# Optimization experiments

Measured on AMD Instinct MI355X. Metric: run time of the kernel, lower is better.

The kernel has to match this reference:

```python
import jax, jax.numpy as jnp
import numpy as np
import math

B, S, D, H, F = 4, 1024, 1024, 16, 4096
NUM_BUCKETS, MAX_DISTANCE = 32, 128
LN_EPS = 1e-5


def _relative_position_bucket(relative_position, num_buckets=NUM_BUCKETS, max_distance=MAX_DISTANCE):
    # bidirectional T5 bucketing, faithful to the torch source
    n = -relative_position
    num_buckets = num_buckets // 2  # 16
    ret = (n < 0).astype(jnp.int32) * num_buckets
    n = jnp.abs(n)
    max_exact = num_buckets // 2  # 8
    is_small = n < max_exact
    val_if_large = max_exact + (
        jnp.log(jnp.maximum(n, 1).astype(jnp.float32) / max_exact)
        / math.log(max_distance / max_exact)
        * (num_buckets - max_exact)
    ).astype(jnp.int32)
    val_if_large = jnp.minimum(val_if_large, num_buckets - 1)
    return ret + jnp.where(is_small, n, val_if_large)


def layer_norm(x, g, b):
    mu = jnp.mean(x, axis=-1, keepdims=True)
    var = jnp.mean((x - mu) ** 2, axis=-1, keepdims=True)
    return g * (x - mu) / jnp.sqrt(var + LN_EPS) + b


def setup_inputs() -> dict:
    key = jax.random.key(0)
    ks = jax.random.split(key, 12)
    s = 0.02
    return {
        "in_state": jax.random.normal(ks[0], (B, S, D), jnp.float32),
        "padding_mask": jnp.ones((B, S), jnp.int32),
        "Wq": jax.random.normal(ks[1], (D, D), jnp.float32) * s,
        "bq": jnp.zeros((D,), jnp.float32),
        "Wk": jax.random.normal(ks[2], (D, D), jnp.float32) * s,
        "bk": jnp.zeros((D,), jnp.float32),
        "Wv": jax.random.normal(ks[3], (D, D), jnp.float32) * s,
        "bv": jnp.zeros((D,), jnp.float32),
        "Wo": jax.random.normal(ks[4], (D, D), jnp.float32) * s,
        "bo": jnp.zeros((D,), jnp.float32),
        "rel_bias": jax.random.normal(ks[5], (NUM_BUCKETS, H), jnp.float32) * s,
        "ln1_g": jnp.ones((D,), jnp.float32),
        "ln1_b": jnp.zeros((D,), jnp.float32),
        "W1": jax.random.normal(ks[6], (D, F), jnp.float32) * s,
        "b1": jnp.zeros((F,), jnp.float32),
        "W2": jax.random.normal(ks[7], (F, D), jnp.float32) * s,
        "b2": jnp.zeros((D,), jnp.float32),
        "ln2_g": jnp.ones((D,), jnp.float32),
        "ln2_b": jnp.zeros((D,), jnp.float32),
    }


def reference(in_state, padding_mask, Wq, bq, Wk, bk, Wv, bv, Wo, bo, rel_bias,
              ln1_g, ln1_b, W1, b1, W2, b2, ln2_g, ln2_b):
    b, s, d = in_state.shape
    dh = d // H
    q = in_state @ Wq + bq
    k = in_state @ Wk + bk
    v = in_state @ Wv + bv
    # faithful to torch's q.view(B*H, S, d_head) flat reshape (no head transpose)
    qh = q.reshape(b * H, s, dh)
    kh = k.reshape(b * H, s, dh)
    vh = v.reshape(b * H, s, dh)
    scores = jnp.einsum('bqd,bkd->bqk', qh, kh)  # no 1/sqrt(d) scaling (T5 style)
    # relative position bias: [H, S, S] tiled over batch -> block index b*H+h gets head h
    rel_pos = jnp.arange(s)[:, None] - jnp.arange(s)[None, :]
    buckets = _relative_position_bucket(rel_pos)
    bias = rel_bias[buckets].transpose(2, 0, 1)  # [H, S, S]
    bias = jnp.tile(bias, (b, 1, 1))  # [B*H, S, S]
    # padding mask: log(0/1) -> -inf/0; block b*H+h uses mask[b, value_index]
    pad = jnp.log(padding_mask.astype(jnp.float32))  # [B, S]
    pad = jnp.repeat(pad, H, axis=0)[:, None, :]  # [B*H, 1, S]
    attw = jax.nn.softmax(scores + bias + pad, axis=-1)
    att = (attw @ vh).reshape(b, s, d)
    att = att @ Wo + bo
    h = layer_norm(att + in_state, ln1_g, ln1_b)
    ff = jnp.maximum(h @ W1 + b1, 0.0) @ W2 + b2
    out = layer_norm(ff + h, ln2_g, ln2_b)
    return out
```

## Files before the change

### kernel.cpp

```cpp
#include <hip/hip_runtime.h>
#include <hip/hip_bf16.h>

typedef unsigned short u16;
typedef __attribute__((ext_vector_type(8))) short bhalf8;
typedef __attribute__((ext_vector_type(4))) float f32x4;

#define DEV __device__ __forceinline__

DEV float bf2f(u16 u) { union { unsigned int i; float f; } c; c.i = ((unsigned int)u) << 16; return c.f; }
DEV u16 f2bf(float f) {
  union { float f; unsigned int i; } c; c.f = f;
  unsigned int x = c.i;
  x += 0x7fffu + ((x >> 16) & 1u);
  return (u16)(x >> 16);
}

DEV void async16(const void* g, void* l) {
  __builtin_amdgcn_global_load_lds((__attribute__((address_space(1))) void*)g,
                                   (__attribute__((address_space(3))) void*)l, 16, 0, 0);
}

struct Ptr11 { const void* p[11]; };
struct TC4 { const void* in[4]; u16* out[4]; };

__global__ void detect_kernel(const unsigned int* __restrict__ x, int* __restrict__ flag) {
  int t = threadIdx.x;
  int cnt = 0;
  for (int i = t; i < 256; i += 64) {
    unsigned int w = x[i];
    int e = (w >> 7) & 0xFF;
    if (e >= 96 && e <= 134) cnt++;
  }
#pragma unroll
  for (int o = 1; o < 64; o <<= 1) cnt += __shfl_xor(cnt, o, 64);
  if (t == 0) *flag = (cnt >= 192) ? 1 : 0;
}

DEV bhalf8 load8B(const void* base, size_t e, int isbf) {
  if (isbf) return *(const bhalf8*)((const u16*)base + e);
  const float* f = (const float*)base + e;
  float4 a = *(const float4*)f;
  float4 b = *(const float4*)(f + 4);
  bhalf8 r;
  r[0] = (short)f2bf(a.x); r[1] = (short)f2bf(a.y); r[2] = (short)f2bf(a.z); r[3] = (short)f2bf(a.w);
  r[4] = (short)f2bf(b.x); r[5] = (short)f2bf(b.y); r[6] = (short)f2bf(b.z); r[7] = (short)f2bf(b.w);
  return r;
}

__global__ __launch_bounds__(256) void convert_x(const void* __restrict__ x,
                                                 u16* __restrict__ dst,
                                                 const int* __restrict__ flag) {
  int c = blockIdx.x * 256 + threadIdx.x;
  u16* d = dst + (size_t)c * 4;
  if (*flag) {
    *(ushort4*)d = ((const ushort4*)x)[c];
  } else {
    float4 v = ((const float4*)x)[c];
    d[0] = f2bf(v.x); d[1] = f2bf(v.y); d[2] = f2bf(v.z); d[3] = f2bf(v.w);
  }
}

__global__ __launch_bounds__(256) void convert_small(Ptr11 s, float* __restrict__ dst,
                                                     const int* __restrict__ flag) {
  const int isbf = *flag;
  const int SZ[11] = {1024,1024,1024,1024,512,1024,1024,4096,1024,1024,1024};
  for (int i = threadIdx.x; i < 13824; i += 256) {
    int acc = 0, seg = -1, off = 0;
#pragma unroll
    for (int s2 = 0; s2 < 11; ++s2) {
      if (seg < 0 && i < acc + SZ[s2]) { seg = s2; off = i - acc; }
      acc += SZ[s2];
    }
    dst[i] = isbf ? bf2f(((const u16*)s.p[seg])[off]) : ((const float*)s.p[seg])[off];
  }
}

DEV void tconv_tile(const void* in, u16* out, int R, int C, int isbf) {
  __shared__ __align__(16) u16 tile[64][72];
  const int t = threadIdx.x;
  const int c0 = blockIdx.x * 64, r0 = blockIdx.y * 64;
#pragma unroll
  for (int r = 0; r < 2; ++r) {
    int idx = r * 256 + t;
    int ri = idx >> 3, cc = (idx & 7) * 8;
    bhalf8 v = load8B(in, (size_t)(r0 + ri) * C + c0 + cc, isbf);
    *(bhalf8*)(&tile[ri][cc]) = v;
  }
  __syncthreads();
#pragma unroll
  for (int r = 0; r < 2; ++r) {
    int idx = r * 256 + t;
    int co = idx >> 3, rc = (idx & 7) * 8;
    bhalf8 v;
#pragma unroll
    for (int ii = 0; ii < 8; ++ii) v[ii] = (short)tile[rc + ii][co];
    *(bhalf8*)(out + (size_t)(c0 + co) * R + r0 + rc) = v;
  }
}

__global__ __launch_bounds__(256) void tconv_w4(TC4 p, const int* __restrict__ flag) {
  int z = blockIdx.z;
  tconv_tile(p.in[z], p.out[z], 1024, 1024, *flag);
}

__global__ __launch_bounds__(256) void tconv_generic(const void* in, u16* out, int R, int C,
                                                     const int* __restrict__ flag) {
  tconv_tile(in, out, R, C, *flag);
}

__global__ __launch_bounds__(256) void transpose_generic(const u16* in, u16* out, int R, int C) {
  __shared__ __align__(16) u16 tile[64][72];
  const int t = threadIdx.x;
  const int c0 = blockIdx.x * 64, r0 = blockIdx.y * 64;
  size_t bs = (size_t)R * C * blockIdx.z;
#pragma unroll
  for (int r = 0; r < 2; ++r) {
    int idx = r * 256 + t;
    int ri = idx >> 3, cc = (idx & 7) * 8;
    *(bhalf8*)(&tile[ri][cc]) = *(const bhalf8*)(in + bs + (size_t)(r0 + ri) * C + c0 + cc);
  }
  __syncthreads();
#pragma unroll
  for (int r = 0; r < 2; ++r) {
    int idx = r * 256 + t;
    int co = idx >> 3, rc = (idx & 7) * 8;
    bhalf8 v;
#pragma unroll
    for (int ii = 0; ii < 8; ++ii) v[ii] = (short)tile[rc + ii][co];
    *(bhalf8*)(out + bs + (size_t)(c0 + co) * R + r0 + rc) = v;
  }
}

#define MFMA_BF16(a, b, c) __builtin_amdgcn_mfma_f32_16x16x32_bf16(a, b, c, 0, 0, 0)

template<int RELU>
__global__ __launch_bounds__(512) void gemm256(
    const u16* __restrict__ A, const u16* __restrict__ BT0,
    const float* __restrict__ b0, const float* __restrict__ b1, const float* __restrict__ b2,
    u16* __restrict__ C0, int M, int N, int K, long sBT, long sC)
{
  __shared__ __align__(16) u16 ldsAll[65536];
  (void)M;

  const int t = threadIdx.x;
  const int wv = t >> 6, l = t & 63;
  const int wm = wv >> 2, wn = wv & 3;
  const int m0 = blockIdx.y * 256, n0 = blockIdx.x * 256;
  const int z = blockIdx.z;

  const u16* BT = BT0 + (long)z * sBT;
  const float* bias = (z == 0) ? b0 : (z == 1 ? b1 : b2);
  u16* C = C0 + (long)z * sC;

  const int ri = t >> 3;
  const int slc8 = (((t & 7) ^ (ri & 7)) << 3);
  const u16* agp = A + (size_t)(m0 + ri) * K + slc8;
  const int rB = ((ri >> 5) << 6) | (ri & 31);
  const u16* bgp = BT + (size_t)(n0 + rB) * K + slc8;

  char* lbase = (char*)ldsAll;
  char* ldst = lbase + wv * 1024;

#define STG_A(bufb, h, j, kt) async16(agp + (size_t)((j) * 128 + (h) * 64) * K + (size_t)(kt) * 64, \
                                      ldst + (bufb) * 32768 + (h) * 16384 + (j) * 8192)
#define STG_B(bufb, h, j, kt) async16(bgp + (size_t)((j) * 128 + (h) * 32) * K + (size_t)(kt) * 64, \
                                      ldst + 65536 + (bufb) * 32768 + (h) * 16384 + (j) * 8192)

  int offA[4][2], offB[2][2];
#pragma unroll
  for (int mi = 0; mi < 4; ++mi)
#pragma unroll
    for (int s = 0; s < 2; ++s)
      offA[mi][s] = wm * 8192 + (mi * 16 + (l & 15)) * 128 + ((((s << 2) + (l >> 4)) ^ (l & 7)) << 4);
#pragma unroll
  for (int nj = 0; nj < 2; ++nj)
#pragma unroll
    for (int s = 0; s < 2; ++s)
      offB[nj][s] = 65536 + wn * 4096 + (nj * 16 + (l & 15)) * 128 + ((((s << 2) + (l >> 4)) ^ (l & 7)) << 4);

  const int NT = K >> 6;
  f32x4 acc[8][4] = {};

  STG_A(0, 0, 0, 0); STG_A(0, 0, 1, 0);
  STG_B(0, 0, 0, 0); STG_B(0, 0, 1, 0);
  STG_B(0, 1, 0, 0); STG_B(0, 1, 1, 0);
  STG_A(0, 1, 0, 0); STG_A(0, 1, 1, 0);
  if (NT > 1) {
    STG_A(1, 0, 0, 1); STG_A(1, 0, 1, 1);
    STG_B(1, 0, 0, 1); STG_B(1, 0, 1, 1);
    STG_B(1, 1, 0, 1); STG_B(1, 1, 1, 1);
    asm volatile("s_waitcnt vmcnt(6)" ::: "memory");
  } else {
    asm volatile("s_waitcnt vmcnt(0)" ::: "memory");
  }
  __builtin_amdgcn_s_barrier();

  for (int tt = 0; tt < NT; ++tt) {
    const int bf = tt & 1;
    const int bo = bf << 15;
    bhalf8 af[4][2], p0[2][2], p1[2][2];

#pragma unroll
    for (int mi = 0; mi < 4; ++mi)
#pragma unroll
      for (int s = 0; s < 2; ++s)
        af[mi][s] = *(const bhalf8*)(lbase + bo + offA[mi][s]);
#pragma unroll
    for (int nj = 0; nj < 2; ++nj)
#pragma unroll
      for (int s = 0; s < 2; ++s)
        p0[nj][s] = *(const bhalf8*)(lbase + bo + offB[nj][s]);
    if (tt + 1 < NT) { STG_A(bf ^ 1, 1, 0, tt + 1); STG_A(bf ^ 1, 1, 1, tt + 1); }
    __builtin_amdgcn_s_barrier();
    asm volatile("s_waitcnt lgkmcnt(0)" ::: "memory");
    __builtin_amdgcn_s_setprio(1);
#pragma unroll
    for (int mi = 0; mi < 4; ++mi)
#pragma unroll
      for (int nj = 0; nj < 2; ++nj) {
        acc[mi][nj] = MFMA_BF16(af[mi][0], p0[nj][0], acc[mi][nj]);
        acc[mi][nj] = MFMA_BF16(af[mi][1], p0[nj][1], acc[mi][nj]);
      }
    __builtin_amdgcn_s_setprio(0);
    __builtin_amdgcn_s_barrier();

#pragma unroll
    for (int nj = 0; nj < 2; ++nj)
#pragma unroll
      for (int s = 0; s < 2; ++s)
        p1[nj][s] = *(const bhalf8*)(lbase + bo + 16384 + offB[nj][s]);
    if (tt + 2 < NT) { STG_A(bf, 0, 0, tt + 2); STG_A(bf, 0, 1, tt + 2); }
    __builtin_amdgcn_s_barrier();
    asm volatile("s_waitcnt lgkmcnt(0)" ::: "memory");
    __builtin_amdgcn_s_setprio(1);
#pragma unroll
    for (int mi = 0; mi < 4; ++mi)
#pragma unroll
      for (int nj = 0; nj < 2; ++nj) {
        acc[mi][2 + nj] = MFMA_BF16(af[mi][0], p1[nj][0], acc[mi][2 + nj]);
        acc[mi][2 + nj] = MFMA_BF16(af[mi][1], p1[nj][1], acc[mi][2 + nj]);
      }
    __builtin_amdgcn_s_setprio(0);
    __builtin_amdgcn_s_barrier();

#pragma unroll
    for (int mi = 0; mi < 4; ++mi)
#pragma unroll
      for (int s = 0; s < 2; ++s)
        af[mi][s] = *(const bhalf8*)(lbase + bo + 16384 + offA[mi][s]);
    if (tt + 2 < NT) { STG_B(bf, 0, 0, tt + 2); STG_B(bf, 0, 1, tt + 2); }
    __builtin_amdgcn_s_barrier();
    asm volatile("s_waitcnt lgkmcnt(0)" ::: "memory");
    __builtin_amdgcn_s_setprio(1);
#pragma unroll
    for (int mi = 0; mi < 4; ++mi)
#pragma unroll
      for (int nj = 0; nj < 2; ++nj) {
        acc[4 + mi][2 + nj] = MFMA_BF16(af[mi][0], p1[nj][0], acc[4 + mi][2 + nj]);
        acc[4 + mi][2 + nj] = MFMA_BF16(af[mi][1], p1[nj][1], acc[4 + mi][2 + nj]);
      }
    __builtin_amdgcn_s_setprio(0);
    __builtin_amdgcn_s_barrier();

    if (tt + 2 < NT) { STG_B(bf, 1, 0, tt + 2); STG_B(bf, 1, 1, tt + 2); }
    __builtin_amdgcn_s_barrier();
    __builtin_amdgcn_s_setprio(1);
#pragma unroll
    for (int mi = 0; mi < 4; ++mi)
#pragma unroll
      for (int nj = 0; nj < 2; ++nj) {
        acc[4 + mi][nj] = MFMA_BF16(af[mi][0], p0[nj][0], acc[4 + mi][nj]);
        acc[4 + mi][nj] = MFMA_BF16(af[mi][1], p0[nj][1], acc[4 + mi][nj]);
      }
    __builtin_amdgcn_s_setprio(0);
    if (tt < NT - 2) {
      asm volatile("s_waitcnt vmcnt(6)" ::: "memory");
    } else if (tt == NT - 2) {
      asm volatile("s_waitcnt vmcnt(0)" ::: "memory");
    }
    __builtin_amdgcn_s_barrier();
  }
#undef STG_A
#undef STG_B

  const int lr = (l >> 4) << 2, lcc = l & 15;
#pragma unroll
  for (int nj = 0; nj < 4; ++nj) {
    int col = n0 + wn * 64 + nj * 16 + lcc;
    float bb = bias[col];
#pragma unroll
    for (int mi = 0; mi < 8; ++mi) {
#pragma unroll
      for (int r = 0; r < 4; ++r) {
        int row = m0 + wm * 128 + mi * 16 + lr + r;
        float v = acc[mi][nj][r] + bb;
        if (RELU) v = fmaxf(v, 0.0f);
        C[(size_t)row * N + col] = f2bf(v);
      }
    }
  }
}

template<int RELU>
__global__ __launch_bounds__(512) void gemm_bt(
    const u16* __restrict__ A, const u16* __restrict__ BT0,
    const float* __restrict__ b0, const float* __restrict__ b1, const float* __restrict__ b2,
    u16* __restrict__ C0, int M, int N, int K, long sBT, long sC)
{
  __shared__ __align__(16) u16 ldsA[128 * 32];
  __shared__ __align__(16) u16 ldsB[128 * 32];

  const int t = threadIdx.x;
  const int wv = t >> 6, l = t & 63;
  const int wm = wv >> 2, wn = wv & 3;
  const int m0 = blockIdx.y * 128, n0 = blockIdx.x * 128;
  const int z = blockIdx.z;

  const u16* BT = BT0 + (long)z * sBT;
  const float* bias = (z == 0) ? b0 : (z == 1 ? b1 : b2);
  u16* C = C0 + (long)z * sC;

  const int mm_s = t >> 2, kc_s = (t & 3) ^ ((t >> 4) & 3);
  const u16* agp = A + (size_t)(m0 + mm_s) * K + kc_s * 8;
  const u16* bgp = BT + (size_t)(n0 + mm_s) * K + kc_s * 8;
  char* la = (char*)ldsA + wv * 1024;
  char* lb = (char*)ldsB + wv * 1024;

  int a_off[4], b_off[2];
#pragma unroll
  for (int i = 0; i < 4; ++i) {
    int mm = wm * 64 + i * 16 + (l & 15);
    a_off[i] = (mm * 4 + ((l >> 4) ^ ((mm >> 2) & 3))) * 8;
  }
#pragma unroll
  for (int j = 0; j < 2; ++j) {
    int nn = wn * 32 + j * 16 + (l & 15);
    b_off[j] = (nn * 4 + ((l >> 4) ^ ((nn >> 2) & 3))) * 8;
  }

  f32x4 acc[4][2] = {};

  for (int kt = 0; kt < K; kt += 32) {
    __syncthreads();
    async16(agp + kt, la);
    async16(bgp + kt, lb);
    __syncthreads();

    bhalf8 af[4], bfr[2];
#pragma unroll
    for (int i = 0; i < 4; ++i) af[i] = *(const bhalf8*)(ldsA + a_off[i]);
#pragma unroll
    for (int j = 0; j < 2; ++j) bfr[j] = *(const bhalf8*)(ldsB + b_off[j]);
#pragma unroll
    for (int mi = 0; mi < 4; ++mi)
#pragma unroll
      for (int nj = 0; nj < 2; ++nj)
        acc[mi][nj] = __builtin_amdgcn_mfma_f32_16x16x32_bf16(af[mi], bfr[nj], acc[mi][nj], 0, 0, 0);
  }

  const int lr = (l >> 4) << 2, lc = l & 15;
#pragma unroll
  for (int nj = 0; nj < 2; ++nj) {
    int col = n0 + wn * 32 + nj * 16 + lc;
    float bb = bias[col];
#pragma unroll
    for (int mi = 0; mi < 4; ++mi) {
#pragma unroll
      for (int r = 0; r < 4; ++r) {
        int row = m0 + wm * 64 + mi * 16 + lr + r;
        float v = acc[mi][nj][r] + bb;
        if (RELU) v = fmaxf(v, 0.0f);
        C[(size_t)row * N + col] = f2bf(v);
      }
    }
  }
}

template<int RELU>
__global__ __launch_bounds__(256) void gemm_bn(
    const u16* __restrict__ A, const void* __restrict__ B,
    const float* __restrict__ bias, u16* __restrict__ C, int M, int N, int K,
    const int* __restrict__ flag)
{
  __shared__ __align__(16) u16 ldsA[128][40];
  __shared__ __align__(16) u16 ldsB[128][40];

  const int isbf = *flag;
  const int t = threadIdx.x;
  const int wv = t >> 6, l = t & 63;
  const int wm = wv & 1, wn = wv >> 1;
  const int m0 = blockIdx.y * 128, n0 = blockIdx.x * 128;

  const int srow = t >> 1, scol = (t & 1) * 16;
  const u16* agp = A + (size_t)(m0 + srow) * K + scol;

  const int kk = t >> 3;
  const int nn = (t & 7) * 16;

  f32x4 acc[4][4] = {};

  for (int kt = 0; kt < K; kt += 32) {
    bhalf8 a0 = *(const bhalf8*)(agp + kt);
    bhalf8 a1 = *(const bhalf8*)(agp + kt + 8);
    size_t e0 = (size_t)(kt + kk) * N + n0 + nn;
    bhalf8 b0v = load8B(B, e0, isbf);
    bhalf8 b1v = load8B(B, e0 + 8, isbf);
    __syncthreads();
    *(bhalf8*)(&ldsA[srow][scol])     = a0;
    *(bhalf8*)(&ldsA[srow][scol + 8]) = a1;
#pragma unroll
    for (int j = 0; j < 8; ++j) ldsB[nn + j][kk]     = (u16)b0v[j];
#pragma unroll
    for (int j = 0; j < 8; ++j) ldsB[nn + 8 + j][kk] = (u16)b1v[j];
    __syncthreads();

    bhalf8 af[4], bfr[4];
#pragma unroll
    for (int i = 0; i < 4; ++i)
      af[i] = *(const bhalf8*)(&ldsA[wm * 64 + i * 16 + (l & 15)][(l >> 4) * 8]);
#pragma unroll
    for (int i = 0; i < 4; ++i)
      bfr[i] = *(const bhalf8*)(&ldsB[wn * 64 + i * 16 + (l & 15)][(l >> 4) * 8]);
#pragma unroll
    for (int mi = 0; mi < 4; ++mi)
#pragma unroll
      for (int ni = 0; ni < 4; ++ni)
        acc[mi][ni] = __builtin_amdgcn_mfma_f32_16x16x32_bf16(af[mi], bfr[ni], acc[mi][ni], 0, 0, 0);
  }

  const int lr = (l >> 4) << 2, lc = l & 15;
#pragma unroll
  for (int ni = 0; ni < 4; ++ni) {
    int col = n0 + wn * 64 + ni * 16 + lc;
    float bb = bias[col];
#pragma unroll
    for (int mi = 0; mi < 4; ++mi) {
#pragma unroll
      for (int r = 0; r < 4; ++r) {
        int row = m0 + wm * 64 + mi * 16 + lr + r;
        float v = acc[mi][ni][r] + bb;
        if (RELU) v = fmaxf(v, 0.0f);
        C[(size_t)row * N + col] = f2bf(v);
      }
    }
  }
}

__global__ __launch_bounds__(256) void lut_kernel(const float* __restrict__ rbc, float* __restrict__ lut) {
  int idx = blockIdx.x * 256 + threadIdx.x;
  if (idx >= 16 * 2047) return;
  int h = idx / 2047;
  int dp = idx - h * 2047;
  int delta = dp - 1023;
  int n = -delta;
  int ret = 0;
  if (n < 0) { ret = 16; n = -n; }
  int bkt;
  if (n < 8) bkt = n;
  else {
    float v = logf((float)n * 0.125f) / logf(16.0f) * 8.0f;
    bkt = 8 + (int)v;
    if (bkt > 15) bkt = 15;
  }
  lut[idx] = (rbc[(ret + bkt) * 16 + h] - 12.0f) * 1.44269504f;
}

__global__ __launch_bounds__(256) void attn_fused(
    const u16* __restrict__ q, const u16* __restrict__ k, const u16* __restrict__ vt,
    const int* __restrict__ mask, const float* __restrict__ lut, u16* __restrict__ att)
{
  __shared__ __align__(16) u16 ldsQ[64][72];
  __shared__ __align__(16) u16 ldsK[64][72];
  __shared__ __align__(16) u16 ldsV[64][72];
  __shared__ __align__(16) u16 ldsP[4][16][72];
  __shared__ float ldsLut[2047];
  __shared__ float ldsPad[64];

  const int t = threadIdx.x;
  const int wv = t >> 6, l = t & 63;
  const int bh = blockIdx.x, qt = blockIdx.y;
  const int b = bh >> 4, h = bh & 15;
  const size_t base = (size_t)bh * 65536;
  const int q0 = qt * 64;

  for (int i = t; i < 2047; i += 256) ldsLut[i] = lut[h * 2047 + i];

  const int sr = t >> 2, sc = (t & 3) * 16;
  {
    bhalf8 q0v = *(const bhalf8*)(q + base + (size_t)(q0 + sr) * 64 + sc);
    bhalf8 q1v = *(const bhalf8*)(q + base + (size_t)(q0 + sr) * 64 + sc + 8);
    *(bhalf8*)(&ldsQ[sr][sc])     = q0v;
    *(bhalf8*)(&ldsQ[sr][sc + 8]) = q1v;
  }
  __syncthreads();

  bhalf8 qf[2];
  {
    int mm = wv * 16 + (l & 15);
#pragma unroll
    for (int s = 0; s < 2; ++s)
      qf[s] = *(const bhalf8*)(&ldsQ[mm][s * 32 + (l >> 4) * 8]);
  }

  float ls_part[4] = {0.0f, 0.0f, 0.0f, 0.0f};
  f32x4 acc_o[4] = {};

  const int* mrow = mask + b * 1024;

  for (int kt = 0; kt < 16; ++kt) {
    const int k0 = kt * 64;
    bhalf8 k0v = *(const bhalf8*)(k + base + (size_t)(k0 + sr) * 64 + sc);
    bhalf8 k1v = *(const bhalf8*)(k + base + (size_t)(k0 + sr) * 64 + sc + 8);
    bhalf8 v0v = *(const bhalf8*)(vt + base + (size_t)sr * 1024 + k0 + sc);
    bhalf8 v1v = *(const bhalf8*)(vt + base + (size_t)sr * 1024 + k0 + sc + 8);
    __syncthreads();
    *(bhalf8*)(&ldsK[sr][sc])     = k0v;
    *(bhalf8*)(&ldsK[sr][sc + 8]) = k1v;
    *(bhalf8*)(&ldsV[sr][sc])     = v0v;
    *(bhalf8*)(&ldsV[sr][sc + 8]) = v1v;
    if (t < 64) {
      int mv = mrow[k0 + t];
      ldsPad[t] = (mv > 0) ? __log2f((float)mv) : -1e30f;
    }
    __syncthreads();

    f32x4 accS[4] = {};
#pragma unroll
    for (int s = 0; s < 2; ++s) {
#pragma unroll
      for (int ni = 0; ni < 4; ++ni) {
        int nnj = ni * 16 + (l & 15);
        bhalf8 kf = *(const bhalf8*)(&ldsK[nnj][s * 32 + (l >> 4) * 8]);
        accS[ni] = __builtin_amdgcn_mfma_f32_16x16x32_bf16(qf[s], kf, accS[ni], 0, 0, 0);
      }
    }

    float padv[4];
#pragma unroll
    for (int ni = 0; ni < 4; ++ni) padv[ni] = ldsPad[ni * 16 + (l & 15)];
    const int ib = q0 + wv * 16 + ((l >> 4) << 2);
#pragma unroll
    for (int r = 0; r < 4; ++r) {
      int i_l = ((l >> 4) << 2) + r;
#pragma unroll
      for (int ni = 0; ni < 4; ++ni) {
        int j_l = ni * 16 + (l & 15);
        float s = fmaf(accS[ni][r], 1.44269504f, ldsLut[(ib + r) - (k0 + j_l) + 1023]) + padv[ni];
        float p = exp2f(s);
        ls_part[r] += p;
        ldsP[wv][i_l][j_l] = f2bf(p);
      }
    }

#pragma unroll
    for (int s = 0; s < 2; ++s) {
      int mm = l & 15;
      bhalf8 pf = *(const bhalf8*)(&ldsP[wv][mm][s * 32 + (l >> 4) * 8]);
#pragma unroll
      for (int ni = 0; ni < 4; ++ni) {
        int e = ni * 16 + (l & 15);
        bhalf8 vf = *(const bhalf8*)(&ldsV[e][s * 32 + (l >> 4) * 8]);
        acc_o[ni] = __builtin_amdgcn_mfma_f32_16x16x32_bf16(pf, vf, acc_o[ni], 0, 0, 0);
      }
    }
  }

#pragma unroll
  for (int r = 0; r < 4; ++r) {
#pragma unroll
    for (int off = 1; off < 16; off <<= 1) ls_part[r] += __shfl_xor(ls_part[r], off, 64);
    ls_part[r] = 1.0f / ls_part[r];
  }

#pragma unroll
  for (int ni = 0; ni < 4; ++ni) {
#pragma unroll
    for (int r = 0; r < 4; ++r) {
      int i = q0 + wv * 16 + ((l >> 4) << 2) + r;
      int e = ni * 16 + (l & 15);
      att[base + (size_t)i * 64 + e] = f2bf(acc_o[ni][r] * ls_part[r]);
    }
  }
}

template<int LAST>
__global__ __launch_bounds__(256) void ln_kernel(
    const u16* __restrict__ x, const u16* __restrict__ res,
    const float* __restrict__ g, const float* __restrict__ b,
    void* __restrict__ out, const int* __restrict__ flag)
{
  const int row = blockIdx.x, t = threadIdx.x;
  const size_t off = (size_t)row * 1024 + t * 4;
  ushort4 xv = *(const ushort4*)(x + off);
  ushort4 rv = *(const ushort4*)(res + off);
  float v0 = bf2f(xv.x) + bf2f(rv.x);
  float v1 = bf2f(xv.y) + bf2f(rv.y);
  float v2 = bf2f(xv.z) + bf2f(rv.z);
  float v3 = bf2f(xv.w) + bf2f(rv.w);
  float s = v0 + v1 + v2 + v3;
  float sq = v0 * v0 + v1 * v1 + v2 * v2 + v3 * v3;
#pragma unroll
  for (int o = 1; o < 64; o <<= 1) { s += __shfl_xor(s, o, 64); sq += __shfl_xor(sq, o, 64); }
  __shared__ float red[8];
  const int wv = t >> 6, l = t & 63;
  if (l == 0) { red[wv] = s; red[4 + wv] = sq; }
  __syncthreads();
  s = red[0] + red[1] + red[2] + red[3];
  sq = red[4] + red[5] + red[6] + red[7];
  float mu = s * 0.0009765625f;
  float var = sq * 0.0009765625f - mu * mu;
  float rstd = rsqrtf(var + 1e-5f);
  float4 gv = *(const float4*)(g + t * 4);
  float4 bv = *(const float4*)(b + t * 4);
  float o0 = gv.x * (v0 - mu) * rstd + bv.x;
  float o1 = gv.y * (v1 - mu) * rstd + bv.y;
  float o2 = gv.z * (v2 - mu) * rstd + bv.z;
  float o3 = gv.w * (v3 - mu) * rstd + bv.w;
  if (!LAST) {
    ushort4 ov; ov.x = f2bf(o0); ov.y = f2bf(o1); ov.z = f2bf(o2); ov.w = f2bf(o3);
    *(ushort4*)((u16*)out + off) = ov;
  } else {
    if (*flag) {
      ushort4 ov; ov.x = f2bf(o0); ov.y = f2bf(o1); ov.z = f2bf(o2); ov.w = f2bf(o3);
      *(ushort4*)((u16*)out + off) = ov;
    } else {
      float4 ov; ov.x = o0; ov.y = o1; ov.z = o2; ov.w = o3;
      *(float4*)((float*)out + off) = ov;
    }
  }
}

extern "C" void kernel_launch(void* const* d_in, const int* in_sizes, int n_in,
                              void* d_out, int out_size, void* d_ws, size_t ws_size,
                              hipStream_t stream) {
  const void* x  = d_in[0];
  const int* mask = (const int*)d_in[1];
  const void* Wq = d_in[2];  const void* bq = d_in[3];
  const void* Wk = d_in[4];  const void* bk = d_in[5];
  const void* Wv = d_in[6];  const void* bv = d_in[7];
  const void* Wo = d_in[8];  const void* bo = d_in[9];
  const void* rb = d_in[10];
  const void* g1 = d_in[11]; const void* be1 = d_in[12];
  const void* W1 = d_in[13]; const void* b1 = d_in[14];
  const void* W2 = d_in[15]; const void* b2 = d_in[16];
  const void* g2 = d_in[17]; const void* be2 = d_in[18];

  char* ws = (char*)d_ws;
  const size_t MB = 1024 * 1024;
  const bool FAST = (ws_size >= 57 * MB);

  const size_t TAIL = FAST ? 56 * MB : 48 * MB;
  float* smalls = (float*)(ws + TAIL);
  float* lut    = (float*)(ws + TAIL + 56 * 1024);
  int*   flag   = (int*)(ws + TAIL + 192 * 1024);

  float* bqc  = smalls + 0;
  float* bkc  = smalls + 1024;
  float* bvc  = smalls + 2048;
  float* boc  = smalls + 3072;
  float* rbc  = smalls + 4096;
  float* g1c  = smalls + 4608;
  float* be1c = smalls + 5632;
  float* b1c  = smalls + 6656;
  float* b2c  = smalls + 10752;
  float* g2c  = smalls + 11776;
  float* be2c = smalls + 12800;

  detect_kernel<<<1, 64, 0, stream>>>((const unsigned int*)x, flag);
  Ptr11 sml;
  sml.p[0] = bq; sml.p[1] = bk; sml.p[2] = bv; sml.p[3] = bo; sml.p[4] = rb;
  sml.p[5] = g1; sml.p[6] = be1; sml.p[7] = b1; sml.p[8] = b2; sml.p[9] = g2; sml.p[10] = be2;
  convert_small<<<1, 256, 0, stream>>>(sml, smalls, flag);
  lut_kernel<<<dim3(128), 256, 0, stream>>>(rbc, lut);

  if (FAST) {
    u16* xc   = (u16*)(ws + 0 * MB);
    u16* WqT  = (u16*)(ws + 8 * MB);
    u16* WkT  = WqT + 1048576;
    u16* WvT  = WqT + 2 * 1048576;
    u16* WoT  = WqT + 3 * 1048576;
    u16* qb   = (u16*)(ws + 16 * MB);
    u16* kb   = (u16*)(ws + 24 * MB);
    u16* vb   = (u16*)(ws + 32 * MB);
    u16* vtb  = (u16*)(ws + 40 * MB);
    u16* attb = (u16*)(ws + 32 * MB);
    u16* xo   = (u16*)(ws + 16 * MB);
    u16* hb   = (u16*)(ws + 48 * MB);
    u16* W1T  = (u16*)(ws + 8 * MB);
    u16* W2T  = (u16*)(ws + 0 * MB);
    u16* ff1  = (u16*)(ws + 16 * MB);
    u16* ff2o = (u16*)(ws + 8 * MB);

    convert_x<<<4096, 256, 0, stream>>>(x, xc, flag);
    TC4 tw; tw.in[0] = Wq; tw.in[1] = Wk; tw.in[2] = Wv; tw.in[3] = Wo;
    tw.out[0] = WqT; tw.out[1] = WkT; tw.out[2] = WvT; tw.out[3] = WoT;
    tconv_w4<<<dim3(16, 16, 4), 256, 0, stream>>>(tw, flag);

    gemm256<0><<<dim3(4, 16, 3), 512, 0, stream>>>(xc, WqT, bqc, bkc, bvc, qb,
                                                   4096, 1024, 1024, 1048576L, 4194304L);
    transpose_generic<<<dim3(1, 16, 64), 256, 0, stream>>>(vb, vtb, 1024, 64);
    attn_fused<<<dim3(64, 16), 256, 0, stream>>>(qb, kb, vtb, mask, lut, attb);
    gemm_bt<0><<<dim3(8, 32, 1), 512, 0, stream>>>(attb, WoT, boc, boc, boc, xo,
                                                   4096, 1024, 1024, 0L, 0L);
    tconv_generic<<<dim3(64, 16), 256, 0, stream>>>(W1, W1T, 1024, 4096, flag);
    ln_kernel<0><<<dim3(4096), 256, 0, stream>>>(xo, xc, g1c, be1c, hb, flag);
    tconv_generic<<<dim3(16, 64), 256, 0, stream>>>(W2, W2T, 4096, 1024, flag);
    gemm256<1><<<dim3(16, 16, 1), 512, 0, stream>>>(hb, W1T, b1c, b1c, b1c, ff1,
                                                    4096, 4096, 1024, 0L, 0L);
    gemm_bt<0><<<dim3(8, 32, 1), 512, 0, stream>>>(ff1, W2T, b2c, b2c, b2c, ff2o,
                                                   4096, 1024, 4096, 0L, 0L);
    ln_kernel<1><<<dim3(4096), 256, 0, stream>>>(ff2o, hb, g2c, be2c, d_out, flag);
  } else {
    u16* xc   = (u16*)(ws + 0 * MB);
    u16* WqT  = (u16*)(ws + 8 * MB);
    u16* WkT  = WqT + 1048576;
    u16* WvT  = WqT + 2 * 1048576;
    u16* WoT  = WqT + 3 * 1048576;
    u16* qb   = (u16*)(ws + 16 * MB);
    u16* kb   = (u16*)(ws + 24 * MB);
    u16* vb   = (u16*)(ws + 32 * MB);
    u16* vtb  = (u16*)(ws + 40 * MB);
    u16* attb = (u16*)(ws + 32 * MB);
    u16* xo   = (u16*)(ws + 16 * MB);
    u16* hb   = (u16*)(ws + 40 * MB);
    u16* ff1  = (u16*)(ws + 0 * MB);
    u16* ff2o = (u16*)(ws + 32 * MB);

    convert_x<<<4096, 256, 0, stream>>>(x, xc, flag);
    TC4 tw; tw.in[0] = Wq; tw.in[1] = Wk; tw.in[2] = Wv; tw.in[3] = Wo;
    tw.out[0] = WqT; tw.out[1] = WkT; tw.out[2] = WvT; tw.out[3] = WoT;
    tconv_w4<<<dim3(16, 16, 4), 256, 0, stream>>>(tw, flag);

    gemm_bt<0><<<dim3(8, 32, 3), 512, 0, stream>>>(xc, WqT, bqc, bkc, bvc, qb,
                                                   4096, 1024, 1024, 1048576L, 4194304L);
    transpose_generic<<<dim3(1, 16, 64), 256, 0, stream>>>(vb, vtb, 1024, 64);
    attn_fused<<<dim3(64, 16), 256, 0, stream>>>(qb, kb, vtb, mask, lut, attb);
    gemm_bt<0><<<dim3(8, 32, 1), 512, 0, stream>>>(attb, WoT, boc, boc, boc, xo,
                                                   4096, 1024, 1024, 0L, 0L);
    ln_kernel<0><<<dim3(4096), 256, 0, stream>>>(xo, xc, g1c, be1c, hb, flag);
    gemm_bn<1><<<dim3(32, 32), 256, 0, stream>>>(hb, W1, b1c, ff1, 4096, 4096, 1024, flag);
    gemm_bn<0><<<dim3(8, 32), 256, 0, stream>>>(ff1, W2, b2c, ff2o, 4096, 1024, 4096, flag);
    ln_kernel<1><<<dim3(4096), 256, 0, stream>>>(ff2o, hb, g2c, be2c, d_out, flag);
  }
}
```

Measured before the change: 436.9 us.

## Split-K the FF2 GEMM with packed bf16 atomics and retile QKV GEMM

The W2 GEMM (K=4096) now runs on the 256x256 tile kernel with a 4-way split-K grid. Partial sums are accumulated into a bf16 output with global_atomic_pk_add_bf16, after a bias_init kernel seeds that output with b2. The QKV projection moves from the 256-tile kernel to the 128-tile gemm_bt kernel, which gives more blocks. The aim is to fill more CUs on the GPU. The trade-offs are extra atomic traffic, a new launch, and bf16 rounding of the accumulated partials, which is nondeterministic in order.

After: 445.1 us. No clear change (+1.9%).

```diff
diff --git a/kernel.cpp b/kernel.cpp
--- a/kernel.cpp
+++ b/kernel.cpp
@@ -18,6 +18,10 @@
 DEV void async16(const void* g, void* l) {
   __builtin_amdgcn_global_load_lds((__attribute__((address_space(1))) void*)g,
                                    (__attribute__((address_space(3))) void*)l, 16, 0, 0);
+}
+
+DEV void atom_pk_bf16(void* p, unsigned int v) {
+  asm volatile("global_atomic_pk_add_bf16 %0, %1, off" :: "v"(p), "v"(v) : "memory");
 }
 
 struct Ptr11 { const void* p[11]; };
@@ -75,6 +79,14 @@
   }
 }
 
+__global__ __launch_bounds__(256) void bias_init(const float* __restrict__ bias,
+                                                 u16* __restrict__ out) {
+  const int row = blockIdx.x, t = threadIdx.x;
+  float4 bv = *(const float4*)(bias + t * 4);
+  ushort4 ov; ov.x = f2bf(bv.x); ov.y = f2bf(bv.y); ov.z = f2bf(bv.z); ov.w = f2bf(bv.w);
+  *(ushort4*)(out + (size_t)row * 1024 + t * 4) = ov;
+}
+
 DEV void tconv_tile(const void* in, u16* out, int R, int C, int isbf) {
   __shared__ __align__(16) u16 tile[64][72];
   const int t = threadIdx.x;
@@ -133,11 +145,11 @@
 
 #define MFMA_BF16(a, b, c) __builtin_amdgcn_mfma_f32_16x16x32_bf16(a, b, c, 0, 0, 0)
 
-template<int RELU>
+template<int RELU, int ATOMIC>
 __global__ __launch_bounds__(512) void gemm256(
     const u16* __restrict__ A, const u16* __restrict__ BT0,
     const float* __restrict__ b0, const float* __restrict__ b1, const float* __restrict__ b2,
-    u16* __restrict__ C0, int M, int N, int K, long sBT, long sC)
+    u16* __restrict__ C0, int M, int N, int ldk, int kext, long sBT, long sC)
 {
   __shared__ __align__(16) u16 ldsAll[65536];
   (void)M;
@@ -148,22 +160,28 @@
   const int m0 = blockIdx.y * 256, n0 = blockIdx.x * 256;
   const int z = blockIdx.z;
 
-  const u16* BT = BT0 + (long)z * sBT;
-  const float* bias = (z == 0) ? b0 : (z == 1 ? b1 : b2);
-  u16* C = C0 + (long)z * sC;
+  const u16* BT; const float* bias; u16* C; int koff;
+  if (ATOMIC) {
+    BT = BT0; bias = b0; C = C0; koff = z * kext;
+  } else {
+    BT = BT0 + (long)z * sBT;
+    bias = (z == 0) ? b0 : (z == 1 ? b1 : b2);
+    C = C0 + (long)z * sC;
+    koff = 0;
+  }
 
   const int ri = t >> 3;
   const int slc8 = (((t & 7) ^ (ri & 7)) << 3);
-  const u16* agp = A + (size_t)(m0 + ri) * K + slc8;
+  const u16* agp = A + (size_t)(m0 + ri) * ldk + koff + slc8;
   const int rB = ((ri >> 5) << 6) | (ri & 31);
-  const u16* bgp = BT + (size_t)(n0 + rB) * K + slc8;
+  const u16* bgp = BT + (size_t)(n0 + rB) * ldk + koff + slc8;
 
   char* lbase = (char*)ldsAll;
   char* ldst = lbase + wv * 1024;
 
-#define STG_A(bufb, h, j, kt) async16(agp + (size_t)((j) * 128 + (h) * 64) * K + (size_t)(kt) * 64, \
+#define STG_A(bufb, h, j, kt) async16(agp + (size_t)((j) * 128 + (h) * 64) * ldk + (size_t)(kt) * 64, \
                                       ldst + (bufb) * 32768 + (h) * 16384 + (j) * 8192)
-#define STG_B(bufb, h, j, kt) async16(bgp + (size_t)((j) * 128 + (h) * 32) * K + (size_t)(kt) * 64, \
+#define STG_B(bufb, h, j, kt) async16(bgp + (size_t)((j) * 128 + (h) * 32) * ldk + (size_t)(kt) * 64, \
                                       ldst + 65536 + (bufb) * 32768 + (h) * 16384 + (j) * 8192)
 
   int offA[4][2], offB[2][2];
@@ -178,7 +196,7 @@
     for (int s = 0; s < 2; ++s)
       offB[nj][s] = 65536 + wn * 4096 + (nj * 16 + (l & 15)) * 128 + ((((s << 2) + (l >> 4)) ^ (l & 7)) << 4);
 
-  const int NT = K >> 6;
+  const int NT = kext >> 6;
   f32x4 acc[8][4] = {};
 
   STG_A(0, 0, 0, 0); STG_A(0, 0, 1, 0);
@@ -284,18 +302,38 @@
 #undef STG_B
 
   const int lr = (l >> 4) << 2, lcc = l & 15;
-#pragma unroll
-  for (int nj = 0; nj < 4; ++nj) {
-    int col = n0 + wn * 64 + nj * 16 + lcc;
-    float bb = bias[col];
-#pragma unroll
-    for (int mi = 0; mi < 8; ++mi) {
-#pragma unroll
-      for (int r = 0; r < 4; ++r) {
-        int row = m0 + wm * 128 + mi * 16 + lr + r;
-        float v = acc[mi][nj][r] + bb;
-        if (RELU) v = fmaxf(v, 0.0f);
-        C[(size_t)row * N + col] = f2bf(v);
+  if (ATOMIC) {
+#pragma unroll
+    for (int nj = 0; nj < 4; ++nj) {
+      int col = n0 + wn * 64 + nj * 16 + lcc;
+#pragma unroll
+      for (int mi = 0; mi < 8; ++mi) {
+#pragma unroll
+        for (int r = 0; r < 4; ++r) {
+          int row = m0 + wm * 128 + mi * 16 + lr + r;
+          float vo = acc[mi][nj][r];
+          float vn = __shfl_xor(vo, 1, 64);
+          if (!(l & 1)) {
+            unsigned int pk = (unsigned int)f2bf(vo) | ((unsigned int)f2bf(vn) << 16);
+            atom_pk_bf16((void*)(C + (size_t)row * N + col), pk);
+          }
+        }
+      }
+    }
+  } else {
+#pragma unroll
+    for (int nj = 0; nj < 4; ++nj) {
+      int col = n0 + wn * 64 + nj * 16 + lcc;
+      float bb = bias[col];
+#pragma unroll
+      for (int mi = 0; mi < 8; ++mi) {
+#pragma unroll
+        for (int r = 0; r < 4; ++r) {
+          int row = m0 + wm * 128 + mi * 16 + lr + r;
+          float v = acc[mi][nj][r] + bb;
+          if (RELU) v = fmaxf(v, 0.0f);
+          C[(size_t)row * N + col] = f2bf(v);
+        }
       }
     }
   }
@@ -696,7 +734,7 @@
     tw.out[0] = WqT; tw.out[1] = WkT; tw.out[2] = WvT; tw.out[3] = WoT;
     tconv_w4<<<dim3(16, 16, 4), 256, 0, stream>>>(tw, flag);
 
-    gemm256<0><<<dim3(4, 16, 3), 512, 0, stream>>>(xc, WqT, bqc, bkc, bvc, qb,
+    gemm_bt<0><<<dim3(8, 32, 3), 512, 0, stream>>>(xc, WqT, bqc, bkc, bvc, qb,
                                                    4096, 1024, 1024, 1048576L, 4194304L);
     transpose_generic<<<dim3(1, 16, 64), 256, 0, stream>>>(vb, vtb, 1024, 64);
     attn_fused<<<dim3(64, 16), 256, 0, stream>>>(qb, kb, vtb, mask, lut, attb);
@@ -705,10 +743,11 @@
     tconv_generic<<<dim3(64, 16), 256, 0, stream>>>(W1, W1T, 1024, 4096, flag);
     ln_kernel<0><<<dim3(4096), 256, 0, stream>>>(xo, xc, g1c, be1c, hb, flag);
     tconv_generic<<<dim3(16, 64), 256, 0, stream>>>(W2, W2T, 4096, 1024, flag);
-    gemm256<1><<<dim3(16, 16, 1), 512, 0, stream>>>(hb, W1T, b1c, b1c, b1c, ff1,
-                                                    4096, 4096, 1024, 0L, 0L);
-    gemm_bt<0><<<dim3(8, 32, 1), 512, 0, stream>>>(ff1, W2T, b2c, b2c, b2c, ff2o,
-                                                   4096, 1024, 4096, 0L, 0L);
+    gemm256<1, 0><<<dim3(16, 16, 1), 512, 0, stream>>>(hb, W1T, b1c, b1c, b1c, ff1,
+                                                       4096, 4096, 1024, 1024, 0L, 0L);
+    bias_init<<<dim3(4096), 256, 0, stream>>>(b2c, ff2o);
+    gemm256<0, 1><<<dim3(4, 16, 4), 512, 0, stream>>>(ff1, W2T, b2c, b2c, b2c, ff2o,
+                                                      4096, 1024, 4096, 1024, 0L, 0L);
     ln_kernel<1><<<dim3(4096), 256, 0, stream>>>(ff2o, hb, g2c, be2c, d_out, flag);
   } else {
     u16* xc   = (u16*)(ws + 0 * MB);
```
